# Kernel tuning notes

Hardware: AMD Instinct MI355X
Metric: run time of the kernel (lower is better)

The kernel has to match this reference:

```python
import jax, jax.numpy as jnp
import numpy as np

OUT, IN, BLK = 11008, 4096, 128

def setup_inputs() -> dict:
    key = jax.random.key(0)
    k1, k2, k3, k4, k5 = jax.random.split(key, 5)
    x = jax.random.normal(k1, (64, IN), dtype=jnp.float32)
    weight = jax.random.randint(k2, (OUT, IN // 2), 0, 256, dtype=jnp.int32)  # packed uint4 pairs
    scale = jax.random.uniform(k3, (OUT, 1, BLK), dtype=jnp.float32) * 0.01 + 1e-4
    zp = jax.random.randint(k4, (OUT, 1, BLK), 0, 16).astype(jnp.float32)
    bias = jax.random.normal(k5, (OUT,), dtype=jnp.float32)
    return {"x": x, "weight": weight, "scale": scale, "zp": zp, "bias": bias}

def reference(x, weight, scale, zp, bias):
    dtype = x.dtype
    # unpack: high nibble first, then low nibble (interleaved along in_features)
    w_h = (weight >> 4) & 15
    w_l = weight & 15
    w_unpacked = jnp.stack((w_h, w_l), axis=-1).reshape(OUT, IN)
    # block-wise dequant: scale/zp shaped [OUT, 1, BLK], broadcast over block index dim
    w_blocked = w_unpacked.reshape(OUT, IN // BLK, BLK).astype(dtype)
    w_rec = ((w_blocked - zp.astype(dtype)) * scale.astype(dtype)).reshape(OUT, IN)
    return x @ w_rec.T + bias
```

## Files before the change

### kernel.cpp

```cpp
#include <hip/hip_runtime.h>

#define OUT_F 11008
#define IN_F  4096
#define PKW   2048
#define BLKQ  128

typedef __attribute__((ext_vector_type(8))) short          s16x8;
typedef __attribute__((ext_vector_type(8))) unsigned short u16x8;
typedef __attribute__((ext_vector_type(4))) float          f32x4;
typedef __attribute__((ext_vector_type(4))) int            i32x4;

__device__ __forceinline__ unsigned short f2bf(float f) {
    union { float f; unsigned u; } v; v.f = f;
    unsigned r = v.u + 0x8000u + ((v.u >> 16) & 1u);
    return (unsigned short)(r >> 16);
}

__global__ void init_out(const float* __restrict__ bias, float* __restrict__ out) {
    int idx = blockIdx.x * 256 + threadIdx.x;
    out[idx] = bias[idx % OUT_F];
}

__global__ void prep_xfrag(const float* __restrict__ x, unsigned short* __restrict__ xf) {
    int kb   = blockIdx.x;
    int t    = threadIdx.x;
    int mt   = t >> 6;
    int lane = t & 63;
    int m  = mt * 16 + (lane & 15);
    int k0 = kb * 32 + (lane >> 4) * 8;
    const float* xp = x + m * IN_F + k0;
    f32x4 a = *(const f32x4*)(xp);
    f32x4 b = *(const f32x4*)(xp + 4);
    u16x8 v;
    v[0] = f2bf(a[0]); v[1] = f2bf(a[1]); v[2] = f2bf(a[2]); v[3] = f2bf(a[3]);
    v[4] = f2bf(b[0]); v[5] = f2bf(b[1]); v[6] = f2bf(b[2]); v[7] = f2bf(b[3]);
    *(u16x8*)(xf + (size_t)((kb * 4 + mt) * 64 + lane) * 8) = v;
}

__global__ __launch_bounds__(256) void qlin_main(
    const int*   __restrict__ wq,
    const float* __restrict__ scale,
    const float* __restrict__ zp,
    const unsigned short* __restrict__ xf,
    float* __restrict__ out)
{
    __shared__ __align__(16) float lf[4096];

    const int t      = threadIdx.x;
    const int oi     = blockIdx.x >> 2;
    const int kc     = blockIdx.x & 3;
    const int o_base = oi * 16;
    const int wave   = t >> 6;
    const int lane   = t & 63;
    const int col16  = lane & 15;
    const int quad   = lane >> 4;
    const int row    = o_base + col16;

    float s[8];
    unsigned zpn;
    {
        const float* sp  = scale + (size_t)row * BLKQ + wave * 32 + quad * 8;
        const float* zpp = zp    + (size_t)row * BLKQ + wave * 32 + quad * 8;
        f32x4 s0 = *(const f32x4*)(sp);
        f32x4 s1 = *(const f32x4*)(sp + 4);
        f32x4 z0 = *(const f32x4*)(zpp);
        f32x4 z1 = *(const f32x4*)(zpp + 4);
        unsigned pk = 0;
        #pragma unroll
        for (int c = 0; c < 4; ++c) {
            s[c]     = s0[c];
            s[4 + c] = s1[c];
            pk |= ((unsigned)z0[c]) << (4 * c);
            pk |= ((unsigned)z1[c]) << (4 * (c + 4));
        }
        zpn = pk;
    }

    const int* wp = wq + (size_t)row * PKW + kc * 512 + wave * 16 + quad * 4;
    const s16x8* xfv = (const s16x8*)xf;
    const int kgb0 = kc * 32 + wave;

    i32x4 wr[8];
    #pragma unroll
    for (int j = 0; j < 8; ++j) wr[j] = *(const i32x4*)(wp + j * 64);

    s16x8 ar[2][4];
    #pragma unroll
    for (int sl = 0; sl < 2; ++sl)
        #pragma unroll
        for (int mt = 0; mt < 4; ++mt)
            ar[sl][mt] = xfv[(size_t)(((kgb0 + 4 * sl) * 4 + mt) * 64 + lane)];

    f32x4 acc[4];
    #pragma unroll
    for (int mt = 0; mt < 4; ++mt) acc[mt] = (f32x4){0.f, 0.f, 0.f, 0.f};

    #pragma unroll
    for (int j = 0; j < 8; ++j) {
        u16x8 ub;
        #pragma unroll
        for (int e = 0; e < 8; ++e) {
            unsigned dw = (unsigned)wr[j][e >> 1];
            int wi = (e & 1) ? (int)(dw & 15u) : (int)((dw >> 4) & 15u);
            int zi = (int)((zpn >> (4 * e)) & 15u);
            ub[e] = f2bf((float)(wi - zi) * s[e]);
        }
        s16x8 bfrag;
        #pragma unroll
        for (int e = 0; e < 8; ++e) bfrag[e] = (short)ub[e];

        #pragma unroll
        for (int mt = 0; mt < 4; ++mt)
            acc[mt] = __builtin_amdgcn_mfma_f32_16x16x32_bf16(ar[j & 1][mt], bfrag, acc[mt], 0, 0, 0);

        if (j < 6) {
            #pragma unroll
            for (int mt = 0; mt < 4; ++mt)
                ar[j & 1][mt] = xfv[(size_t)(((kgb0 + 4 * (j + 2)) * 4 + mt) * 64 + lane)];
        }
    }

    #pragma unroll
    for (int mt = 0; mt < 4; ++mt) {
        #pragma unroll
        for (int r = 0; r < 4; ++r) {
            int m = mt * 16 + quad * 4 + r;
            lf[wave * 1024 + m * 16 + col16] = acc[mt][r];
        }
    }
    __syncthreads();
    #pragma unroll
    for (int p = 0; p < 4; ++p) {
        int e = p * 256 + t;
        int m = e >> 4, col = e & 15;
        float v = lf[e] + lf[1024 + e] + lf[2048 + e] + lf[3072 + e];
        atomicAdd(&out[(size_t)m * OUT_F + o_base + col], v);
    }
}

extern "C" void kernel_launch(void* const* d_in, const int* in_sizes, int n_in,
                              void* d_out, int out_size, void* d_ws, size_t ws_size,
                              hipStream_t stream) {
    const float* x     = (const float*)d_in[0];
    const int*   wq    = (const int*)d_in[1];
    const float* scale = (const float*)d_in[2];
    const float* zpv   = (const float*)d_in[3];
    const float* bias  = (const float*)d_in[4];
    float* out = (float*)d_out;
    unsigned short* xf = (unsigned short*)d_ws;

    init_out<<<(64 * OUT_F) / 256, 256, 0, stream>>>(bias, out);
    prep_xfrag<<<128, 256, 0, stream>>>(x, xf);
    qlin_main<<<(OUT_F / 16) * 4, 256, 0, stream>>>(wq, scale, zpv, xf, out);
}
```

Measured before the change: 172.0 us.

## Stage weights through LDS with async double-buffered loads and wider output tiles

Weight tiles are now copied with global_load_lds async copies into a double-buffered, padded shared-memory region and prefetched one K step ahead. Each block covers 32 output rows and half of K instead of 16 rows and a quarter, so every loaded x fragment feeds twice as many MFMAs and half as many atomic partial sums are written. The aim is to hide weight-fetch latency and cut redundant x loads and atomic traffic. In exchange the kernel launches fewer blocks, uses more LDS and registers, and adds barriers inside the loop.

Result: faster. 161.4 us (-6.2%).

```diff
diff --git a/kernel.cpp b/kernel.cpp
--- a/kernel.cpp
+++ b/kernel.cpp
@@ -4,6 +4,9 @@
 #define IN_F  4096
 #define PKW   2048
 #define BLKQ  128
+
+#define PAIR_STRIDE 1056
+#define BUF_BYTES   (16 * PAIR_STRIDE)
 
 typedef __attribute__((ext_vector_type(8))) short          s16x8;
 typedef __attribute__((ext_vector_type(8))) unsigned short u16x8;
@@ -14,6 +17,13 @@
     union { float f; unsigned u; } v; v.f = f;
     unsigned r = v.u + 0x8000u + ((v.u >> 16) & 1u);
     return (unsigned short)(r >> 16);
+}
+
+__device__ __forceinline__ void async_copy16(const void* g, void* l) {
+    __builtin_amdgcn_global_load_lds(
+        (const __attribute__((address_space(1))) void*)g,
+        (__attribute__((address_space(3))) void*)l,
+        16, 0, 0);
 }
 
 __global__ void init_out(const float* __restrict__ bias, float* __restrict__ out) {
@@ -44,21 +54,23 @@
     const unsigned short* __restrict__ xf,
     float* __restrict__ out)
 {
-    __shared__ __align__(16) float lf[4096];
+    __shared__ __align__(16) unsigned char smem[2 * BUF_BYTES];
 
     const int t      = threadIdx.x;
-    const int oi     = blockIdx.x >> 2;
-    const int kc     = blockIdx.x & 3;
-    const int o_base = oi * 16;
+    const int oi     = blockIdx.x >> 1;
+    const int kc     = blockIdx.x & 1;
+    const int o_base = oi * 32;
     const int wave   = t >> 6;
     const int lane   = t & 63;
     const int col16  = lane & 15;
     const int quad   = lane >> 4;
-    const int row    = o_base + col16;
+    const int l5     = lane & 31;
 
-    float s[8];
-    unsigned zpn;
-    {
+    float s[2][8];
+    unsigned zpn[2];
+    #pragma unroll
+    for (int oh = 0; oh < 2; ++oh) {
+        int row = o_base + oh * 16 + col16;
         const float* sp  = scale + (size_t)row * BLKQ + wave * 32 + quad * 8;
         const float* zpp = zp    + (size_t)row * BLKQ + wave * 32 + quad * 8;
         f32x4 s0 = *(const f32x4*)(sp);
@@ -68,74 +80,103 @@
         unsigned pk = 0;
         #pragma unroll
         for (int c = 0; c < 4; ++c) {
-            s[c]     = s0[c];
-            s[4 + c] = s1[c];
+            s[oh][c]     = s0[c];
+            s[oh][4 + c] = s1[c];
             pk |= ((unsigned)z0[c]) << (4 * c);
             pk |= ((unsigned)z1[c]) << (4 * (c + 4));
         }
-        zpn = pk;
+        zpn[oh] = pk;
     }
 
-    const int* wp = wq + (size_t)row * PKW + kc * 512 + wave * 16 + quad * 4;
     const s16x8* xfv = (const s16x8*)xf;
-    const int kgb0 = kc * 32 + wave;
 
-    i32x4 wr[8];
+    #define STAGE(rr, b) do {                                                   \
+        const unsigned int* g0 = (const unsigned int*)wq                        \
+            + (size_t)(o_base + wave * 8 + (lane >> 5)) * PKW                   \
+            + kc * 1024 + (rr) * 128 + l5 * 4;                                  \
+        unsigned char* lb = smem + (b) * BUF_BYTES + wave * 4 * PAIR_STRIDE;    \
+        _Pragma("unroll")                                                       \
+        for (int i_ = 0; i_ < 4; ++i_)                                          \
+            async_copy16(g0 + (size_t)i_ * 2 * PKW, lb + i_ * PAIR_STRIDE);     \
+    } while (0)
+
+    f32x4 acc[2][4];
     #pragma unroll
-    for (int j = 0; j < 8; ++j) wr[j] = *(const i32x4*)(wp + j * 64);
+    for (int oh = 0; oh < 2; ++oh)
+        #pragma unroll
+        for (int mt = 0; mt < 4; ++mt) acc[oh][mt] = (f32x4){0.f, 0.f, 0.f, 0.f};
 
-    s16x8 ar[2][4];
+    STAGE(0, 0);
+    __syncthreads();
+
+    for (int rr = 0; rr < 8; ++rr) {
+        const unsigned char* buf = smem + (rr & 1) * BUF_BYTES;
+
+        s16x8 ar[2][4];
+        #pragma unroll
+        for (int ii = 0; ii < 2; ++ii) {
+            int kb = kc * 64 + rr * 8 + wave + 4 * ii;
+            #pragma unroll
+            for (int mt = 0; mt < 4; ++mt)
+                ar[ii][mt] = xfv[(size_t)((kb * 4 + mt) * 64 + lane)];
+        }
+
+        if (rr < 7) STAGE(rr + 1, (rr + 1) & 1);
+
+        #pragma unroll
+        for (int ii = 0; ii < 2; ++ii) {
+            int iw = wave + 4 * ii;
+            #pragma unroll
+            for (int oh = 0; oh < 2; ++oh) {
+                int rowl = oh * 16 + col16;
+                const unsigned char* baddr = buf + (rowl >> 1) * PAIR_STRIDE
+                                           + (rowl & 1) * 512 + iw * 64 + quad * 16;
+                i32x4 raw = *(const i32x4*)baddr;
+                u16x8 ub;
+                #pragma unroll
+                for (int e = 0; e < 8; ++e) {
+                    unsigned dw = (unsigned)raw[e >> 1];
+                    int wi = (e & 1) ? (int)(dw & 15u) : (int)((dw >> 4) & 15u);
+                    int zi = (int)((zpn[oh] >> (4 * e)) & 15u);
+                    ub[e] = f2bf((float)(wi - zi) * s[oh][e]);
+                }
+                s16x8 bfrag;
+                #pragma unroll
+                for (int e = 0; e < 8; ++e) bfrag[e] = (short)ub[e];
+
+                #pragma unroll
+                for (int mt = 0; mt < 4; ++mt)
+                    acc[oh][mt] = __builtin_amdgcn_mfma_f32_16x16x32_bf16(
+                        ar[ii][mt], bfrag, acc[oh][mt], 0, 0, 0);
+            }
+        }
+
+        __syncthreads();
+    }
+
+    float* lf = (float*)smem;
     #pragma unroll
-    for (int sl = 0; sl < 2; ++sl)
+    for (int oh = 0; oh < 2; ++oh)
         #pragma unroll
         for (int mt = 0; mt < 4; ++mt)
-            ar[sl][mt] = xfv[(size_t)(((kgb0 + 4 * sl) * 4 + mt) * 64 + lane)];
-
-    f32x4 acc[4];
-    #pragma unroll
-    for (int mt = 0; mt < 4; ++mt) acc[mt] = (f32x4){0.f, 0.f, 0.f, 0.f};
-
-    #pragma unroll
-    for (int j = 0; j < 8; ++j) {
-        u16x8 ub;
-        #pragma unroll
-        for (int e = 0; e < 8; ++e) {
-            unsigned dw = (unsigned)wr[j][e >> 1];
-            int wi = (e & 1) ? (int)(dw & 15u) : (int)((dw >> 4) & 15u);
-            int zi = (int)((zpn >> (4 * e)) & 15u);
-            ub[e] = f2bf((float)(wi - zi) * s[e]);
-        }
-        s16x8 bfrag;
-        #pragma unroll
-        for (int e = 0; e < 8; ++e) bfrag[e] = (short)ub[e];
-
-        #pragma unroll
-        for (int mt = 0; mt < 4; ++mt)
-            acc[mt] = __builtin_amdgcn_mfma_f32_16x16x32_bf16(ar[j & 1][mt], bfrag, acc[mt], 0, 0, 0);
-
-        if (j < 6) {
             #pragma unroll
-            for (int mt = 0; mt < 4; ++mt)
-                ar[j & 1][mt] = xfv[(size_t)(((kgb0 + 4 * (j + 2)) * 4 + mt) * 64 + lane)];
-        }
-    }
-
-    #pragma unroll
-    for (int mt = 0; mt < 4; ++mt) {
-        #pragma unroll
-        for (int r = 0; r < 4; ++r) {
-            int m = mt * 16 + quad * 4 + r;
-            lf[wave * 1024 + m * 16 + col16] = acc[mt][r];
-        }
-    }
+            for (int r = 0; r < 4; ++r) {
+                int m16 = quad * 4 + r;
+                int e = ((oh * 4 + mt) * 16 + m16) * 16 + col16;
+                lf[wave * 2048 + e] = acc[oh][mt][r];
+            }
     __syncthreads();
     #pragma unroll
-    for (int p = 0; p < 4; ++p) {
+    for (int p = 0; p < 8; ++p) {
         int e = p * 256 + t;
-        int m = e >> 4, col = e & 15;
-        float v = lf[e] + lf[1024 + e] + lf[2048 + e] + lf[3072 + e];
-        atomicAdd(&out[(size_t)m * OUT_F + o_base + col], v);
+        int col = e & 15, m16 = (e >> 4) & 15, c2 = e >> 8;
+        int oh = c2 >> 2, mt = c2 & 3;
+        int m = mt * 16 + m16;
+        int o = o_base + oh * 16 + col;
+        float v = lf[e] + lf[2048 + e] + lf[4096 + e] + lf[6144 + e];
+        atomicAdd(&out[(size_t)m * OUT_F + o], v);
     }
+    #undef STAGE
 }
 
 extern "C" void kernel_launch(void* const* d_in, const int* in_sizes, int n_in,
@@ -151,5 +192,5 @@
 
     init_out<<<(64 * OUT_F) / 256, 256, 0, stream>>>(bias, out);
     prep_xfrag<<<128, 256, 0, stream>>>(x, xf);
-    qlin_main<<<(OUT_F / 16) * 4, 256, 0, stream>>>(wq, scale, zpv, xf, out);
+    qlin_main<<<(OUT_F / 32) * 2, 256, 0, stream>>>(wq, scale, zpv, xf, out);
 }
```
